# Kernel optimization log

Measured on AMD Instinct MI355X. Metric: run time of the kernel, lower is better.

## Reference

```python
import jax, jax.numpy as jnp
import numpy as np

N = 10000        # nodes
E = 320000       # edges (before self-loops)
IN = 128         # in_channels
HID = 128        # hidden_channels per head
HEADS = 4
OUT = 512        # out_channels (final layer, 1 head, no concat)
SLOPE = 0.2      # PyG GATConv negative_slope default


def setup_inputs() -> dict:
    key = jax.random.key(0)
    ks = jax.random.split(key, 16)
    s = 0.05
    inp = {
        "x": jax.random.normal(ks[0], (N, IN), dtype=jnp.float32),
        "edge_index": jax.random.randint(ks[1], (2, E), 0, N, dtype=jnp.int32),
        # layer 1: IN -> HEADS*HID, concat
        "W1": jax.random.normal(ks[2], (IN, HEADS * HID), dtype=jnp.float32) * s,
        "a_src1": jax.random.normal(ks[3], (1, HEADS, HID), dtype=jnp.float32) * s,
        "a_dst1": jax.random.normal(ks[4], (1, HEADS, HID), dtype=jnp.float32) * s,
        "b1": jnp.zeros((HEADS * HID,), dtype=jnp.float32),
        # layer 2: HEADS*HID -> HEADS*HID, concat
        "W2": jax.random.normal(ks[5], (HEADS * HID, HEADS * HID), dtype=jnp.float32) * s,
        "a_src2": jax.random.normal(ks[6], (1, HEADS, HID), dtype=jnp.float32) * s,
        "a_dst2": jax.random.normal(ks[7], (1, HEADS, HID), dtype=jnp.float32) * s,
        "b2": jnp.zeros((HEADS * HID,), dtype=jnp.float32),
        # layer 3: HEADS*HID -> OUT, heads=1, mean (no concat)
        "W3": jax.random.normal(ks[8], (HEADS * HID, OUT), dtype=jnp.float32) * s,
        "a_src3": jax.random.normal(ks[9], (1, 1, OUT), dtype=jnp.float32) * s,
        "a_dst3": jax.random.normal(ks[10], (1, 1, OUT), dtype=jnp.float32) * s,
        "b3": jnp.zeros((OUT,), dtype=jnp.float32),
    }
    return inp


def gat_layer(x, src, dst, W, a_src, a_dst, bias, heads, ch, concat):
    n = x.shape[0]
    h = (x @ W).reshape(n, heads, ch)                 # [N,H,C]
    al_s = jnp.sum(h * a_src, axis=-1)                # [N,H]
    al_d = jnp.sum(h * a_dst, axis=-1)                # [N,H]
    logits = jax.nn.leaky_relu(al_s[src] + al_d[dst], SLOPE)  # [E,H]
    # segment softmax over incoming edges of each destination node
    logits = logits - jax.ops.segment_max(logits, dst, num_segments=n)[dst]
    e = jnp.exp(logits)
    denom = jax.ops.segment_sum(e, dst, num_segments=n)[dst]
    alpha = e / denom                                  # [E,H]
    out = jax.ops.segment_sum(h[src] * alpha[:, :, None], dst, num_segments=n)  # [N,H,C]
    out = out.reshape(n, heads * ch) if concat else out.mean(axis=1)
    return out + bias


def reference(x, edge_index, W1, a_src1, a_dst1, b1, W2, a_src2, a_dst2, b2,
              W3, a_src3, a_dst3, b3):
    n = x.shape[0]
    loop = jnp.arange(n, dtype=edge_index.dtype)       # PyG add_self_loops=True
    src = jnp.concatenate([edge_index[0], loop])
    dst = jnp.concatenate([edge_index[1], loop])
    h = jax.nn.relu(gat_layer(x, src, dst, W1, a_src1, a_dst1, b1, HEADS, HID, True))
    h = jax.nn.relu(gat_layer(h, src, dst, W2, a_src2, a_dst2, b2, HEADS, HID, True))
    return gat_layer(h, src, dst, W3, a_src3, a_dst3, b3, 1, OUT, False)
```

## Files before the change

### kernel.cpp

```cpp
#include <hip/hip_runtime.h>

#define NSLOPE 0.2f
#define CAP 128

typedef __bf16 bf16x8 __attribute__((ext_vector_type(8)));
typedef __bf16 bf16x4 __attribute__((ext_vector_type(4)));
typedef __bf16 bf16x2 __attribute__((ext_vector_type(2)));
typedef float  f32x4  __attribute__((ext_vector_type(4)));


__global__ void fill_kernel(const int* __restrict__ ei, int E,
                            int* cnt, int* __restrict__ col){
  int i = blockIdx.x*blockDim.x + threadIdx.x;
  if (i < E){
    int s = ei[i], d = ei[E + i];
    int slot = atomicAdd(&cnt[d], 1);
    if (slot < CAP) col[(d << 7) + slot] = s;
  }
}

__device__ __forceinline__ void wsplit_body(
    const float* __restrict__ W, __bf16* __restrict__ Bt, int K, int Nc,
    int kb, int nb, float (*hi_s)[33], float (*lo_s)[33]){
  int tx = threadIdx.x & 31, ty = threadIdx.x >> 5;
  int k0 = kb * 32, n0 = nb * 32;
#pragma unroll
  for (int i = 0; i < 4; i++){
    int r = ty + i*8;
    float v = W[(size_t)(k0 + r)*Nc + n0 + tx];
    float h = (float)(__bf16)v;
    hi_s[r][tx] = h;
    lo_s[r][tx] = v - h;
  }
  __syncthreads();
  const size_t K2x16 = (size_t)(2*K) * 16;
  const size_t lo_off = (size_t)(K >> 5) * 512;
#pragma unroll
  for (int i = 0; i < 4; i++){
    int n = ty + i*8;
    int r = n0 + n;
    size_t a = (size_t)(r >> 4)*K2x16 + (size_t)(k0 >> 5)*512
             + (size_t)((r & 15) + 16*(tx >> 3))*8 + (tx & 7);
    Bt[a]          = (__bf16)hi_s[tx][n];
    Bt[a + lo_off] = (__bf16)lo_s[tx][n];
  }
}

__global__ __launch_bounds__(256) void prep_kernel(
    const float* __restrict__ x, __bf16* __restrict__ X2,
    const float* __restrict__ W1, __bf16* __restrict__ B1t,
    const float* __restrict__ W2, __bf16* __restrict__ B2t,
    const float* __restrict__ W3, __bf16* __restrict__ B3t,
    int* __restrict__ cnt, int* __restrict__ col,
    float* __restrict__ albase, int N){
  __shared__ float hi_s[32][33], lo_s[32][33];
  int b = blockIdx.x, t = threadIdx.x;
  int gid = b*256 + t;
  if (gid < N){
    cnt[gid] = 1;
    col[gid << 7] = gid;
  }
  if (gid*4 < N*18) *(float4*)(albase + gid*4) = make_float4(0.f,0.f,0.f,0.f);

  const int nb_split = (N*32 + 255) / 256;
  if (b < nb_split){
    int i = gid * 4;
    if (i < N*128){
      int n = i >> 7, c = i & 127;
      float4 v = *(const float4*)(x + i);
      float f[4] = {v.x, v.y, v.z, v.w};
      bf16x4 h, l;
#pragma unroll
      for (int u = 0; u < 4; u++){
        __bf16 hh = (__bf16)f[u];
        h[u] = hh;
        l[u] = (__bf16)(f[u] - (float)hh);
      }
      size_t a = (size_t)(n >> 4)*4096 + (size_t)(c >> 5)*512
               + (size_t)((n & 15) + 16*((c >> 3) & 3))*8 + (c & 7);
      *(bf16x4*)(X2 + a)        = h;
      *(bf16x4*)(X2 + a + 2048) = l;
    }
  } else if (b < nb_split + 64){
    int bb = b - nb_split;
    wsplit_body(W1, B1t, 128, 512, bb & 3, bb >> 2, hi_s, lo_s);
  } else if (b < nb_split + 64 + 256){
    int bb = b - nb_split - 64;
    wsplit_body(W2, B2t, 512, 512, bb & 15, bb >> 4, hi_s, lo_s);
  } else {
    int bb = b - nb_split - 320;
    wsplit_body(W3, B3t, 512, 512, bb & 15, bb >> 4, hi_s, lo_s);
  }
}

template<int H>
__global__ __launch_bounds__(256) void gemm_mfma(
    const __bf16* __restrict__ A2f, const __bf16* __restrict__ B2f,
    __bf16* __restrict__ Hb, const float* __restrict__ asrc,
    const float* __restrict__ adst, float* __restrict__ al_s,
    float* __restrict__ al_d, int M, int K2){
  int t = threadIdx.x, w = t >> 6, lane = t & 63;
  int mm = lane & 15, q = lane >> 4;

  int bid = blockIdx.x;
  int idx = bid >> 3;
  int cb = idx & 3;
  int rowblk = (bid & 7) + ((idx >> 2) << 3);
  if (rowblk * 64 >= M) return;
  int bm = rowblk * 64, bn = cb * 128;
  int wr = w & 1, wc = w >> 1;

  const int nf = K2 >> 5;
  const int rbmax = (M >> 4) - 1;
  const __bf16* pA0; const __bf16* pA1;
  const __bf16* pB0; const __bf16* pB1; const __bf16* pB2; const __bf16* pB3;
  {
    int rb0 = (bm >> 4) + wr*2;     rb0 = (rb0 <= rbmax) ? rb0 : rbmax;
    int rb1 = (bm >> 4) + wr*2 + 1; rb1 = (rb1 <= rbmax) ? rb1 : rbmax;
    pA0 = A2f + (size_t)rb0*nf*512 + lane*8;
    pA1 = A2f + (size_t)rb1*nf*512 + lane*8;
    int rbB = (bn >> 4) + wc*4;
    pB0 = B2f + (size_t)(rbB+0)*nf*512 + lane*8;
    pB1 = B2f + (size_t)(rbB+1)*nf*512 + lane*8;
    pB2 = B2f + (size_t)(rbB+2)*nf*512 + lane*8;
    pB3 = B2f + (size_t)(rbB+3)*nf*512 + lane*8;
  }

  f32x4 acc[2][4];
#pragma unroll
  for (int i = 0; i < 2; i++)
#pragma unroll
    for (int j = 0; j < 4; j++)
#pragma unroll
      for (int r = 0; r < 4; r++) acc[i][j][r] = 0.f;

#pragma unroll 4
  for (int f = 0; f < nf; f++){
    bf16x8 a0 = *(const bf16x8*)(pA0 + (size_t)f*512);
    bf16x8 a1 = *(const bf16x8*)(pA1 + (size_t)f*512);
    bf16x8 b0 = *(const bf16x8*)(pB0 + (size_t)f*512);
    bf16x8 b1 = *(const bf16x8*)(pB1 + (size_t)f*512);
    bf16x8 b2 = *(const bf16x8*)(pB2 + (size_t)f*512);
    bf16x8 b3 = *(const bf16x8*)(pB3 + (size_t)f*512);
    acc[0][0] = __builtin_amdgcn_mfma_f32_16x16x32_bf16(a0, b0, acc[0][0], 0, 0, 0);
    acc[0][1] = __builtin_amdgcn_mfma_f32_16x16x32_bf16(a0, b1, acc[0][1], 0, 0, 0);
    acc[0][2] = __builtin_amdgcn_mfma_f32_16x16x32_bf16(a0, b2, acc[0][2], 0, 0, 0);
    acc[0][3] = __builtin_amdgcn_mfma_f32_16x16x32_bf16(a0, b3, acc[0][3], 0, 0, 0);
    acc[1][0] = __builtin_amdgcn_mfma_f32_16x16x32_bf16(a1, b0, acc[1][0], 0, 0, 0);
    acc[1][1] = __builtin_amdgcn_mfma_f32_16x16x32_bf16(a1, b1, acc[1][1], 0, 0, 0);
    acc[1][2] = __builtin_amdgcn_mfma_f32_16x16x32_bf16(a1, b2, acc[1][2], 0, 0, 0);
    acc[1][3] = __builtin_amdgcn_mfma_f32_16x16x32_bf16(a1, b3, acc[1][3], 0, 0, 0);
  }

  float as_v[4], ad_v[4];
#pragma unroll
  for (int j2 = 0; j2 < 4; j2++){
    int colc = bn + (wc*4 + j2)*16 + mm;
    as_v[j2] = asrc[colc];
    ad_v[j2] = adst[colc];
  }
  const int h = (H == 4) ? (bn >> 7) : 0;
#pragma unroll
  for (int i2 = 0; i2 < 2; i2++){
    int rbase = bm + (wr*2 + i2)*16 + q*4;
#pragma unroll
    for (int j2 = 0; j2 < 4; j2++){
      int colc = bn + (wc*4 + j2)*16 + mm;
#pragma unroll
      for (int r = 0; r < 4; r++){
        int row = rbase + r;
        if (row < M) Hb[(size_t)row*512 + colc] = (__bf16)acc[i2][j2][r];
      }
    }
#pragma unroll
    for (int r = 0; r < 4; r++){
      float ps = acc[i2][0][r]*as_v[0] + acc[i2][1][r]*as_v[1]
               + acc[i2][2][r]*as_v[2] + acc[i2][3][r]*as_v[3];
      float pd = acc[i2][0][r]*ad_v[0] + acc[i2][1][r]*ad_v[1]
               + acc[i2][2][r]*ad_v[2] + acc[i2][3][r]*ad_v[3];
#pragma unroll
      for (int off = 1; off < 16; off <<= 1){
        ps += __shfl_xor(ps, off);
        pd += __shfl_xor(pd, off);
      }
      int row = rbase + r;
      if (mm == 0 && row < M){
        atomicAdd(&al_s[(size_t)row*H + h], ps);
        atomicAdd(&al_d[(size_t)row*H + h], pd);
      }
    }
  }
}

template<int H, int MODE>
__global__ __launch_bounds__(64) void aggregate_slice(
    const __bf16* __restrict__ Hb, const float* __restrict__ al_s,
    const float* __restrict__ al_d, const int* __restrict__ cnt,
    const int* __restrict__ col, const float* __restrict__ bias,
    float* __restrict__ outF, __bf16* __restrict__ fA,
    int nidx, int N){
  int g = blockIdx.x;
  int x = g & 7, idx = g >> 3;
  int s = x >> 1, half = x & 1;
  int d = half * nidx + idx;
  if (d >= N) return;
  int lane = threadIdx.x;
  int start = d << 7;
  int end = start + cnt[d];
  const int hh = (H == 1) ? 0 : s;
  const float ald = al_d[(size_t)d*H + hh];
  const bf16x2* __restrict__ Hb2 = (const bf16x2*)Hb;
  const size_t coff = s*64 + lane;

  float mx = -1e30f;
  for (int e = start + lane; e < end; e += 64){
    int sc = col[e];
    float v = al_s[(size_t)sc*H + hh] + ald;
    v = (v > 0.f) ? v : NSLOPE * v;
    mx = fmaxf(mx, v);
  }
#pragma unroll
  for (int off = 32; off > 0; off >>= 1)
    mx = fmaxf(mx, __shfl_xor(mx, off));

  __shared__ int   src_s[64];
  __shared__ float a_s[64];

  float ax0=0.f, ay0=0.f, ax1=0.f, ay1=0.f;
  float ax2=0.f, ay2=0.f, ax3=0.f, ay3=0.f;
  float lsum = 0.f;

  for (int c0 = start; c0 < end; c0 += 64){
    int cnt2 = min(64, end - c0);
    if (lane < cnt2){
      int e = c0 + lane;
      int sc = col[e];
      float v = al_s[(size_t)sc*H + hh] + ald;
      v = (v > 0.f) ? v : NSLOPE * v;
      float ev = __expf(v - mx);
      src_s[lane] = sc;
      a_s[lane]   = ev;
      lsum += ev;
    }
    __syncthreads();
    int i = 0;
    for (; i + 4 <= cnt2; i += 4){
      int s0 = src_s[i],   s1 = src_s[i+1];
      int s2 = src_s[i+2], s3 = src_s[i+3];
      float e0 = a_s[i],   e1 = a_s[i+1];
      float e2 = a_s[i+2], e3 = a_s[i+3];
      bf16x2 v0 = Hb2[(size_t)s0*256 + coff];
      bf16x2 v1 = Hb2[(size_t)s1*256 + coff];
      bf16x2 v2 = Hb2[(size_t)s2*256 + coff];
      bf16x2 v3 = Hb2[(size_t)s3*256 + coff];
      ax0 += e0*(float)v0[0]; ay0 += e0*(float)v0[1];
      ax1 += e1*(float)v1[0]; ay1 += e1*(float)v1[1];
      ax2 += e2*(float)v2[0]; ay2 += e2*(float)v2[1];
      ax3 += e3*(float)v3[0]; ay3 += e3*(float)v3[1];
    }
    for (; i < cnt2; i++){
      int s0 = src_s[i];
      float e0 = a_s[i];
      bf16x2 v0 = Hb2[(size_t)s0*256 + coff];
      ax0 += e0*(float)v0[0]; ay0 += e0*(float)v0[1];
    }
    __syncthreads();
  }

#pragma unroll
  for (int off = 32; off > 0; off >>= 1)
    lsum += __shfl_xor(lsum, off);

  float accx = (ax0 + ax1) + (ax2 + ax3);
  float accy = (ay0 + ay1) + (ay2 + ay3);
  float invd = 1.f / lsum;
  int c = s*128 + lane*2;
  float2 bv = *(const float2*)(bias + c);
  float r0 = accx * invd + bv.x;
  float r1 = accy * invd + bv.y;
  if (MODE == 1){
    r0 = fmaxf(r0, 0.f); r1 = fmaxf(r1, 0.f);
    __bf16 h0 = (__bf16)r0, h1 = (__bf16)r1;
    bf16x2 hv; hv[0] = h0; hv[1] = h1;
    bf16x2 lv; lv[0] = (__bf16)(r0 - (float)h0); lv[1] = (__bf16)(r1 - (float)h1);
    size_t a = (size_t)(d >> 4)*16384 + (size_t)(c >> 5)*512
             + (size_t)((d & 15) + 16*((c >> 3) & 3))*8 + (c & 7);
    *(bf16x2*)(fA + a)        = hv;
    *(bf16x2*)(fA + a + 8192) = lv;
  } else {
    *(float2*)(outF + (size_t)d*512 + c) = make_float2(r0, r1);
  }
}

extern "C" void kernel_launch(void* const* d_in, const int* in_sizes, int n_in,
                              void* d_out, int out_size, void* d_ws, size_t ws_size,
                              hipStream_t stream){
  const float* x   = (const float*)d_in[0];
  const int*   ei  = (const int*)  d_in[1];
  const float* W1  = (const float*)d_in[2];
  const float* as1 = (const float*)d_in[3];
  const float* ad1 = (const float*)d_in[4];
  const float* b1  = (const float*)d_in[5];
  const float* W2  = (const float*)d_in[6];
  const float* as2 = (const float*)d_in[7];
  const float* ad2 = (const float*)d_in[8];
  const float* b2  = (const float*)d_in[9];
  const float* W3  = (const float*)d_in[10];
  const float* as3 = (const float*)d_in[11];
  const float* ad3 = (const float*)d_in[12];
  const float* b3  = (const float*)d_in[13];
  float* out = (float*)d_out;

  const int N = in_sizes[0] / 128;
  const int E = in_sizes[1] / 2;
  const int nidx = (N + 1) / 2;

  __bf16* feat2  = (__bf16*)d_ws;
  __bf16* X2     = feat2 + (size_t)N*1024;
  float*  albase = (float*)(X2 + (size_t)N*256);
  float*  als1   = albase;
  float*  ald1   = als1 + (size_t)N*4;
  float*  als2   = ald1 + (size_t)N*4;
  float*  ald2   = als2 + (size_t)N*4;
  float*  als3   = ald2 + (size_t)N*4;
  float*  ald3   = als3 + (size_t)N;
  int*    cnt    = (int*)(ald3 + (size_t)N);
  int*    col    = cnt + N;
  uintptr_t p  = (uintptr_t)(col + (size_t)N*CAP);
  p = (p + 15) & ~(uintptr_t)15;
  __bf16* B1t = (__bf16*)p;
  __bf16* B2t = B1t + 512*256;
  __bf16* B3t = B2t + 512*1024;
  __bf16* Hb  = B3t + 512*1024;

  const int nb_split = (N*32 + 255)/256;
  const int pgrid = nb_split + 64 + 256 + 256;

  prep_kernel<<<pgrid, 256, 0, stream>>>(x, X2, W1, B1t, W2, B2t, W3, B3t,
                                         cnt, col, albase, N);
  fill_kernel<<<(E+255)/256, 256, 0, stream>>>(ei, E, cnt, col);

  const int nrb = (N + 63)/64;
  const int ggrid = (((nrb + 7) >> 3) << 3) * 4;
  const int agrid = nidx * 8;

  gemm_mfma<4><<<ggrid, 256, 0, stream>>>(X2, B1t, Hb, as1, ad1, als1, ald1, N, 256);
  aggregate_slice<4,1><<<agrid, 64, 0, stream>>>(Hb, als1, ald1, cnt, col, b1,
      (float*)nullptr, feat2, nidx, N);

  gemm_mfma<4><<<ggrid, 256, 0, stream>>>(feat2, B2t, Hb, as2, ad2, als2, ald2, N, 1024);
  aggregate_slice<4,1><<<agrid, 64, 0, stream>>>(Hb, als2, ald2, cnt, col, b2,
      (float*)nullptr, feat2, nidx, N);

  gemm_mfma<1><<<ggrid, 256, 0, stream>>>(feat2, B3t, Hb, as3, ad3, als3, ald3, N, 1024);
  aggregate_slice<1,0><<<agrid, 64, 0, stream>>>(Hb, als3, ald3, cnt, col, b3,
      out, (__bf16*)nullptr, nidx, N);
}
```

Measured before the change: 304.9 us.

## Use fp16 features with fdot2 aggregation and one 256-thread block per node

The intermediate projected features are stored as fp16 instead of bf16, and the aggregation kernel uses packed fp16 dot2 instructions over pairs of edges, with attention weights also held in fp16. The aggregation launch now uses one 256-thread block per destination node, one wave per head slice, instead of 64-thread blocks. Edge logits are loaded once into registers (up to 128 edges), which removes the separate max pass and the block-level syncs. This gives up some precision because fp16 attention weights and features are used, and fp16 can overflow where bf16 would not.

```diff
diff --git a/kernel.cpp b/kernel.cpp
--- a/kernel.cpp
+++ b/kernel.cpp
@@ -7,6 +7,17 @@
 typedef __bf16 bf16x4 __attribute__((ext_vector_type(4)));
 typedef __bf16 bf16x2 __attribute__((ext_vector_type(2)));
 typedef float  f32x4  __attribute__((ext_vector_type(4)));
+typedef _Float16 half2v __attribute__((ext_vector_type(2)));
+
+static __device__ __forceinline__ float dot2f(unsigned p, unsigned a, float c){
+#if __has_builtin(__builtin_amdgcn_fdot2)
+  return __builtin_amdgcn_fdot2(__builtin_bit_cast(half2v, p),
+                                __builtin_bit_cast(half2v, a), c, false);
+#else
+  half2v ph = __builtin_bit_cast(half2v, p), ah = __builtin_bit_cast(half2v, a);
+  return c + (float)ph[0]*(float)ah[0] + (float)ph[1]*(float)ah[1];
+#endif
+}
 
 
 __global__ void fill_kernel(const int* __restrict__ ei, int E,
@@ -96,7 +107,7 @@
 template<int H>
 __global__ __launch_bounds__(256) void gemm_mfma(
     const __bf16* __restrict__ A2f, const __bf16* __restrict__ B2f,
-    __bf16* __restrict__ Hb, const float* __restrict__ asrc,
+    _Float16* __restrict__ Hb, const float* __restrict__ asrc,
     const float* __restrict__ adst, float* __restrict__ al_s,
     float* __restrict__ al_d, int M, int K2){
   int t = threadIdx.x, w = t >> 6, lane = t & 63;
@@ -169,7 +180,7 @@
 #pragma unroll
       for (int r = 0; r < 4; r++){
         int row = rbase + r;
-        if (row < M) Hb[(size_t)row*512 + colc] = (__bf16)acc[i2][j2][r];
+        if (row < M) Hb[(size_t)row*512 + colc] = (_Float16)acc[i2][j2][r];
       }
     }
 #pragma unroll
@@ -193,88 +204,99 @@
 }
 
 template<int H, int MODE>
-__global__ __launch_bounds__(64) void aggregate_slice(
-    const __bf16* __restrict__ Hb, const float* __restrict__ al_s,
+__global__ __launch_bounds__(256) void aggregate_slice(
+    const _Float16* __restrict__ Hb, const float* __restrict__ al_s,
     const float* __restrict__ al_d, const int* __restrict__ cnt,
     const int* __restrict__ col, const float* __restrict__ bias,
-    float* __restrict__ outF, __bf16* __restrict__ fA,
-    int nidx, int N){
-  int g = blockIdx.x;
-  int x = g & 7, idx = g >> 3;
-  int s = x >> 1, half = x & 1;
-  int d = half * nidx + idx;
+    float* __restrict__ outF, __bf16* __restrict__ fA, int N){
+  __shared__ int      src_s[4][64];
+  __shared__ _Float16 a_sh[4][64];
+  int d = blockIdx.x;
   if (d >= N) return;
-  int lane = threadIdx.x;
+  int t = threadIdx.x, w = t >> 6, lane = t & 63;
+  const int hh = (H == 1) ? 0 : w;
+  const float ald = al_d[(size_t)d*H + hh];
+  int deg = cnt[d]; deg = (deg < CAP) ? deg : CAP;
   int start = d << 7;
-  int end = start + cnt[d];
-  const int hh = (H == 1) ? 0 : s;
-  const float ald = al_d[(size_t)d*H + hh];
-  const bf16x2* __restrict__ Hb2 = (const bf16x2*)Hb;
-  const size_t coff = s*64 + lane;
-
-  float mx = -1e30f;
-  for (int e = start + lane; e < end; e += 64){
-    int sc = col[e];
-    float v = al_s[(size_t)sc*H + hh] + ald;
-    v = (v > 0.f) ? v : NSLOPE * v;
-    mx = fmaxf(mx, v);
-  }
+
+  int sc0 = 0, sc1 = 0;
+  float v0f = -1e30f, v1f = -1e30f;
+  if (lane < deg){
+    sc0 = col[start + lane];
+    float v = al_s[(size_t)sc0*H + hh] + ald;
+    v0f = (v > 0.f) ? v : NSLOPE * v;
+  }
+  if (64 + lane < deg){
+    sc1 = col[start + 64 + lane];
+    float v = al_s[(size_t)sc1*H + hh] + ald;
+    v1f = (v > 0.f) ? v : NSLOPE * v;
+  }
+  float mx = fmaxf(v0f, v1f);
 #pragma unroll
   for (int off = 32; off > 0; off >>= 1)
     mx = fmaxf(mx, __shfl_xor(mx, off));
 
-  __shared__ int   src_s[64];
-  __shared__ float a_s[64];
-
-  float ax0=0.f, ay0=0.f, ax1=0.f, ay1=0.f;
-  float ax2=0.f, ay2=0.f, ax3=0.f, ay3=0.f;
-  float lsum = 0.f;
-
-  for (int c0 = start; c0 < end; c0 += 64){
-    int cnt2 = min(64, end - c0);
-    if (lane < cnt2){
-      int e = c0 + lane;
-      int sc = col[e];
-      float v = al_s[(size_t)sc*H + hh] + ald;
-      v = (v > 0.f) ? v : NSLOPE * v;
-      float ev = __expf(v - mx);
-      src_s[lane] = sc;
-      a_s[lane]   = ev;
-      lsum += ev;
-    }
-    __syncthreads();
-    int i = 0;
-    for (; i + 4 <= cnt2; i += 4){
-      int s0 = src_s[i],   s1 = src_s[i+1];
-      int s2 = src_s[i+2], s3 = src_s[i+3];
-      float e0 = a_s[i],   e1 = a_s[i+1];
-      float e2 = a_s[i+2], e3 = a_s[i+3];
-      bf16x2 v0 = Hb2[(size_t)s0*256 + coff];
-      bf16x2 v1 = Hb2[(size_t)s1*256 + coff];
-      bf16x2 v2 = Hb2[(size_t)s2*256 + coff];
-      bf16x2 v3 = Hb2[(size_t)s3*256 + coff];
-      ax0 += e0*(float)v0[0]; ay0 += e0*(float)v0[1];
-      ax1 += e1*(float)v1[0]; ay1 += e1*(float)v1[1];
-      ax2 += e2*(float)v2[0]; ay2 += e2*(float)v2[1];
-      ax3 += e3*(float)v3[0]; ay3 += e3*(float)v3[1];
-    }
-    for (; i < cnt2; i++){
-      int s0 = src_s[i];
-      float e0 = a_s[i];
-      bf16x2 v0 = Hb2[(size_t)s0*256 + coff];
-      ax0 += e0*(float)v0[0]; ay0 += e0*(float)v0[1];
-    }
-    __syncthreads();
-  }
-
+  float e0 = (lane < deg)      ? __expf(v0f - mx) : 0.f;
+  float e1 = (64 + lane < deg) ? __expf(v1f - mx) : 0.f;
+  float lsum = e0 + e1;
 #pragma unroll
   for (int off = 32; off > 0; off >>= 1)
     lsum += __shfl_xor(lsum, off);
 
-  float accx = (ax0 + ax1) + (ax2 + ax3);
-  float accy = (ay0 + ay1) + (ay2 + ay3);
+  const unsigned* __restrict__ Hb32 = (const unsigned*)Hb;
+  const unsigned coffu = w*64 + lane;
+  float accx = 0.f, accy = 0.f;
+
+  int cc0 = (deg < 64) ? deg : 64;
+  src_s[w][lane] = sc0;
+  a_sh[w][lane]  = (_Float16)e0;
+  for (int chunk = 0; ; chunk++){
+    int cnt2 = (chunk == 0) ? cc0 : (deg - 64);
+    int npair = cnt2 >> 1;
+    int j = 0;
+    for (; j + 2 <= npair; j += 2){
+      int s0 = src_s[w][2*j],     s1 = src_s[w][2*j+1];
+      int s2 = src_s[w][2*j+2],   s3 = src_s[w][2*j+3];
+      unsigned a01 = *(const unsigned*)&a_sh[w][2*j];
+      unsigned a23 = *(const unsigned*)&a_sh[w][2*j+2];
+      unsigned u0 = Hb32[(size_t)s0*256 + coffu];
+      unsigned u1 = Hb32[(size_t)s1*256 + coffu];
+      unsigned u2 = Hb32[(size_t)s2*256 + coffu];
+      unsigned u3 = Hb32[(size_t)s3*256 + coffu];
+      unsigned pc  = (u0 & 0x0000ffffu) | (u1 << 16);
+      unsigned pc1 = (u0 >> 16) | (u1 & 0xffff0000u);
+      unsigned qc  = (u2 & 0x0000ffffu) | (u3 << 16);
+      unsigned qc1 = (u2 >> 16) | (u3 & 0xffff0000u);
+      accx = dot2f(pc,  a01, accx);
+      accy = dot2f(pc1, a01, accy);
+      accx = dot2f(qc,  a23, accx);
+      accy = dot2f(qc1, a23, accy);
+    }
+    for (; j < npair; j++){
+      int s0 = src_s[w][2*j], s1 = src_s[w][2*j+1];
+      unsigned a01 = *(const unsigned*)&a_sh[w][2*j];
+      unsigned u0 = Hb32[(size_t)s0*256 + coffu];
+      unsigned u1 = Hb32[(size_t)s1*256 + coffu];
+      unsigned pc  = (u0 & 0x0000ffffu) | (u1 << 16);
+      unsigned pc1 = (u0 >> 16) | (u1 & 0xffff0000u);
+      accx = dot2f(pc,  a01, accx);
+      accy = dot2f(pc1, a01, accy);
+    }
+    if (cnt2 & 1){
+      int sl = src_s[w][cnt2 - 1];
+      float al = (float)a_sh[w][cnt2 - 1];
+      unsigned ul = Hb32[(size_t)sl*256 + coffu];
+      half2v hv = __builtin_bit_cast(half2v, ul);
+      accx += al * (float)hv[0];
+      accy += al * (float)hv[1];
+    }
+    if (chunk == 1 || deg <= 64) break;
+    src_s[w][lane] = sc1;
+    a_sh[w][lane]  = (_Float16)e1;
+  }
+
   float invd = 1.f / lsum;
-  int c = s*128 + lane*2;
+  int c = w*128 + lane*2;
   float2 bv = *(const float2*)(bias + c);
   float r0 = accx * invd + bv.x;
   float r1 = accy * invd + bv.y;
@@ -313,7 +335,6 @@
 
   const int N = in_sizes[0] / 128;
   const int E = in_sizes[1] / 2;
-  const int nidx = (N + 1) / 2;
 
   __bf16* feat2  = (__bf16*)d_ws;
   __bf16* X2     = feat2 + (size_t)N*1024;
@@ -331,7 +352,7 @@
   __bf16* B1t = (__bf16*)p;
   __bf16* B2t = B1t + 512*256;
   __bf16* B3t = B2t + 512*1024;
-  __bf16* Hb  = B3t + 512*1024;
+  _Float16* Hb = (_Float16*)(B3t + 512*1024);
 
   const int nb_split = (N*32 + 255)/256;
   const int pgrid = nb_split + 64 + 256 + 256;
@@ -342,17 +363,16 @@
 
   const int nrb = (N + 63)/64;
   const int ggrid = (((nrb + 7) >> 3) << 3) * 4;
-  const int agrid = nidx * 8;
 
   gemm_mfma<4><<<ggrid, 256, 0, stream>>>(X2, B1t, Hb, as1, ad1, als1, ald1, N, 256);
-  aggregate_slice<4,1><<<agrid, 64, 0, stream>>>(Hb, als1, ald1, cnt, col, b1,
-      (float*)nullptr, feat2, nidx, N);
+  aggregate_slice<4,1><<<N, 256, 0, stream>>>(Hb, als1, ald1, cnt, col, b1,
+      (float*)nullptr, feat2, N);
 
   gemm_mfma<4><<<ggrid, 256, 0, stream>>>(feat2, B2t, Hb, as2, ad2, als2, ald2, N, 1024);
-  aggregate_slice<4,1><<<agrid, 64, 0, stream>>>(Hb, als2, ald2, cnt, col, b2,
-      (float*)nullptr, feat2, nidx, N);
+  aggregate_slice<4,1><<<N, 256, 0, stream>>>(Hb, als2, ald2, cnt, col, b2,
+      (float*)nullptr, feat2, N);
 
   gemm_mfma<1><<<ggrid, 256, 0, stream>>>(feat2, B3t, Hb, as3, ad3, als3, ald3, N, 1024);
-  aggregate_slice<1,0><<<agrid, 64, 0, stream>>>(Hb, als3, ald3, cnt, col, b3,
-      out, (__bf16*)nullptr, nidx, N);
-}
+  aggregate_slice<1,0><<<N, 256, 0, stream>>>(Hb, als3, ald3, cnt, col, b3,
+      out, (__bf16*)nullptr, N);
+}
```

Result: slower. 335.3 us (+10.0%).
